# Kernel optimization log

Measured on AMD Instinct MI355X. Metric: run time of the kernel, lower is better.

## Reference

```python
import jax, jax.numpy as jnp
import numpy as np

B = 524288        # batch
W = 64            # window_size


def setup_inputs() -> dict:
    key = jax.random.key(0)
    k1, k2, k3 = jax.random.split(key, 3)
    x = jax.random.normal(k1, (B, W), dtype=jnp.float32)
    theta = 0.01 * jax.random.normal(k2, (W, 2), dtype=jnp.float32)
    w = jax.random.normal(k3, (1, 1), dtype=jnp.float32)
    b = jnp.zeros((1,), dtype=jnp.float32)
    return {"x": x, "theta": theta, "w": w, "b": b}


def _expval_z(x, theta):
    """Single-qubit re-uploading circuit: for each t, RX(x_t) RY(th_t0) RZ(th_t1)
    applied to |0>, then <Z>. State carried as two complex amplitudes [B]."""
    bsz = x.shape[0]
    s0 = jnp.ones((bsz,), dtype=jnp.complex64)
    s1 = jnp.zeros((bsz,), dtype=jnp.complex64)

    def step(state, inp):
        s0, s1 = state
        xt, th = inp                      # xt: [B], th: [2]
        # RX(xt): [[c, -i s], [-i s, c]], half-angle
        c = jnp.cos(0.5 * xt).astype(jnp.complex64)
        s = jnp.sin(0.5 * xt).astype(jnp.complex64)
        n0 = c * s0 - 1j * s * s1
        n1 = -1j * s * s0 + c * s1
        # RY(th[0]): [[cy, -sy], [sy, cy]]
        cy = jnp.cos(0.5 * th[0]).astype(jnp.complex64)
        sy = jnp.sin(0.5 * th[0]).astype(jnp.complex64)
        m0 = cy * n0 - sy * n1
        m1 = sy * n0 + cy * n1
        # RZ(th[1]): diag(e^{-i th/2}, e^{+i th/2})
        p = jnp.exp(-0.5j * th[1].astype(jnp.complex64))
        return (p * m0, jnp.conj(p) * m1), None

    (s0, s1), _ = jax.lax.scan(step, (s0, s1), (x.T, theta))  # xs leading dim W
    # <Z> = |s0|^2 - |s1|^2 (real)
    return ((s0 * jnp.conj(s0) - s1 * jnp.conj(s1)).real).astype(jnp.float32)


def reference(x, theta, w, b):
    z = _expval_z(x, theta)               # [B]
    return z * w[0, 0] + b[0]             # Linear(1,1) readout, squeezed -> [B]
```

## Files before the change

### kernel.cpp

```cpp
#include <hip/hip_runtime.h>

#define WSZ    64
#define BLOCK  256
#define INV2PI 0.15915494309189535f

__global__ __launch_bounds__(BLOCK) void sq_main(
    const float* __restrict__ x,
    const float* __restrict__ theta,
    const float* __restrict__ w,
    const float* __restrict__ bias,
    float* __restrict__ out)
{
    __shared__ float4 tA[WSZ];
    __shared__ float4 tB[WSZ];

    const int tid = threadIdx.x;
    const size_t row = (size_t)blockIdx.x * BLOCK + tid;
    const float4* xr4 = reinterpret_cast<const float4*>(x + row * WSZ);

    const float wv = w[0];
    const float bv = bias[0];

    float4 bufA[4], bufB[4];

    auto issue = [&](float4 (&b)[4], int g) {
        #pragma unroll
        for (int k = 0; k < 4; ++k) b[k] = xr4[g * 4 + k];
    };

    issue(bufA, 0);
    issue(bufB, 1);

    if (tid < WSZ) {
        float2 th = reinterpret_cast<const float2*>(theta)[tid];
        float sa = __builtin_amdgcn_sinf(th.x * INV2PI);
        float ca = __builtin_amdgcn_cosf(th.x * INV2PI);
        float sb = __builtin_amdgcn_sinf(th.y * INV2PI);
        float cb = __builtin_amdgcn_cosf(th.y * INV2PI);
        tA[tid] = make_float4(cb * ca, -sb, cb * sa, sb * ca);
        tB[tid] = make_float4(cb, sb * sa, -sa, ca);
    }
    __syncthreads();

    float vx = 0.0f, vy = 0.0f, vz = 1.0f;

    auto quarter = [&](float4 (&b)[4], int g) {
        __builtin_amdgcn_sched_barrier(0);
        #pragma unroll
        for (int c = 0; c < 4; ++c) {
            float q[4] = {b[c].x, b[c].y, b[c].z, b[c].w};
            #pragma unroll
            for (int j = 0; j < 4; ++j) {
                const int t = g * 16 + c * 4 + j;
                float r  = q[j] * INV2PI;
                float s  = __builtin_amdgcn_sinf(r);
                float co = __builtin_amdgcn_cosf(r);
                float4 A  = tA[t];
                float4 Bv = tB[t];
                float y1 = co * vy - s  * vz;
                float z1 = s  * vy + co * vz;
                float nx = A.x  * vx + A.y  * y1 + A.z  * z1;
                float ny = A.w  * vx + Bv.x * y1 + Bv.y * z1;
                float nz = Bv.z * vx + Bv.w * z1;
                vx = nx; vy = ny; vz = nz;
            }
        }
    };

    quarter(bufA, 0);
    issue(bufA, 2);
    quarter(bufB, 1);
    issue(bufB, 3);
    quarter(bufA, 2);
    quarter(bufB, 3);

    out[row] = vz * wv + bv;
}

extern "C" void kernel_launch(void* const* d_in, const int* in_sizes, int n_in,
                              void* d_out, int out_size, void* d_ws, size_t ws_size,
                              hipStream_t stream) {
    const float* x     = (const float*)d_in[0];
    const float* theta = (const float*)d_in[1];
    const float* w     = (const float*)d_in[2];
    const float* b     = (const float*)d_in[3];
    float* out = (float*)d_out;

    int nrows = out_size;
    int grid  = nrows / BLOCK;
    sq_main<<<grid, BLOCK, 0, stream>>>(x, theta, w, b, out);
}
```

Measured before the change: 38.25 us.

## Precompute theta rotation coefficients in a separate kernel and read via scalar loads

Moves the per-window theta rotation matrix computation out of every block into a tiny pre-kernel that writes the coefficients to workspace. The main kernel then reads them through the constant address space so they become uniform scalar loads, dropping the LDS table, the per-block trig work and the __syncthreads. In exchange it adds a second kernel launch and a dependency between the two kernels, and it relies on the scalar loads being hoisted or cached.

```diff
diff --git a/kernel.cpp b/kernel.cpp
--- a/kernel.cpp
+++ b/kernel.cpp
@@ -4,19 +4,31 @@
 #define BLOCK  256
 #define INV2PI 0.15915494309189535f
 
+typedef const __attribute__((address_space(4))) float cfloat;
+
+__global__ void coef_kernel(const float* __restrict__ theta, float* __restrict__ coef) {
+    int t = threadIdx.x;
+    float2 th = reinterpret_cast<const float2*>(theta)[t];
+    float sa = __builtin_amdgcn_sinf(th.x * INV2PI);
+    float ca = __builtin_amdgcn_cosf(th.x * INV2PI);
+    float sb = __builtin_amdgcn_sinf(th.y * INV2PI);
+    float cb = __builtin_amdgcn_cosf(th.y * INV2PI);
+    float4* c4 = reinterpret_cast<float4*>(coef);
+    c4[2 * t + 0] = make_float4(cb * ca, -sb, cb * sa, sb * ca);
+    c4[2 * t + 1] = make_float4(cb, sb * sa, -sa, ca);
+}
+
 __global__ __launch_bounds__(BLOCK) void sq_main(
     const float* __restrict__ x,
-    const float* __restrict__ theta,
+    const float* __restrict__ coef,
     const float* __restrict__ w,
     const float* __restrict__ bias,
     float* __restrict__ out)
 {
-    __shared__ float4 tA[WSZ];
-    __shared__ float4 tB[WSZ];
-
     const int tid = threadIdx.x;
     const size_t row = (size_t)blockIdx.x * BLOCK + tid;
     const float4* xr4 = reinterpret_cast<const float4*>(x + row * WSZ);
+    cfloat* cf = (cfloat*)coef;
 
     const float wv = w[0];
     const float bv = bias[0];
@@ -31,17 +43,6 @@
     issue(bufA, 0);
     issue(bufB, 1);
 
-    if (tid < WSZ) {
-        float2 th = reinterpret_cast<const float2*>(theta)[tid];
-        float sa = __builtin_amdgcn_sinf(th.x * INV2PI);
-        float ca = __builtin_amdgcn_cosf(th.x * INV2PI);
-        float sb = __builtin_amdgcn_sinf(th.y * INV2PI);
-        float cb = __builtin_amdgcn_cosf(th.y * INV2PI);
-        tA[tid] = make_float4(cb * ca, -sb, cb * sa, sb * ca);
-        tB[tid] = make_float4(cb, sb * sa, -sa, ca);
-    }
-    __syncthreads();
-
     float vx = 0.0f, vy = 0.0f, vz = 1.0f;
 
     auto quarter = [&](float4 (&b)[4], int g) {
@@ -52,16 +53,15 @@
             #pragma unroll
             for (int j = 0; j < 4; ++j) {
                 const int t = g * 16 + c * 4 + j;
+                cfloat* m = cf + t * 8;
                 float r  = q[j] * INV2PI;
                 float s  = __builtin_amdgcn_sinf(r);
                 float co = __builtin_amdgcn_cosf(r);
-                float4 A  = tA[t];
-                float4 Bv = tB[t];
                 float y1 = co * vy - s  * vz;
                 float z1 = s  * vy + co * vz;
-                float nx = A.x  * vx + A.y  * y1 + A.z  * z1;
-                float ny = A.w  * vx + Bv.x * y1 + Bv.y * z1;
-                float nz = Bv.z * vx + Bv.w * z1;
+                float nx = m[0] * vx + m[1] * y1 + m[2] * z1;
+                float ny = m[3] * vx + m[4] * y1 + m[5] * z1;
+                float nz = m[6] * vx + m[7] * z1;
                 vx = nx; vy = ny; vz = nz;
             }
         }
@@ -84,9 +84,12 @@
     const float* theta = (const float*)d_in[1];
     const float* w     = (const float*)d_in[2];
     const float* b     = (const float*)d_in[3];
-    float* out = (float*)d_out;
+    float* out  = (float*)d_out;
+    float* coef = (float*)d_ws;
+
+    coef_kernel<<<1, WSZ, 0, stream>>>(theta, coef);
 
     int nrows = out_size;
     int grid  = nrows / BLOCK;
-    sq_main<<<grid, BLOCK, 0, stream>>>(x, theta, w, b, out);
+    sq_main<<<grid, BLOCK, 0, stream>>>(x, coef, w, b, out);
 }
```

New measurement: 39.93 us. +4.4%, slower.
